# Kernel optimization log

Measured on AMD Instinct MI355X. Metric: run time of the kernel, lower is better.

Reference implementation:

```python
import jax, jax.numpy as jnp
import numpy as np

B, L, D, H = 2, 256, 256, 4
DH = D // H  # 64


def setup_inputs() -> dict:
    key = jax.random.key(0)
    ks = jax.random.split(key, 20)
    inp = {
        "q": jax.random.normal(ks[0], (B, L, D), jnp.float32),
        "k": jax.random.normal(ks[1], (B, L, D), jnp.float32),
        "v": jax.random.normal(ks[2], (B, L, D), jnp.float32),
        "attn_mask": jnp.zeros((L, L), jnp.float32),  # nonzero => masked
        "key_padding_mask": jnp.zeros((B, L), bool),
        "pitch_rel": jax.random.normal(ks[3], (B, L, L, D), jnp.float32),
        "dur_rel": jax.random.normal(ks[4], (B, L, L, D), jnp.float32),
    }
    scale = 1.0 / np.sqrt(D)
    names = ["Wq", "Wk", "Wv", "fc", "pr", "dr"]
    for i, n in enumerate(names):
        inp[n + "_w"] = jax.random.normal(ks[5 + 2 * i], (D, D), jnp.float32) * scale
        inp[n + "_b"] = jax.random.normal(ks[6 + 2 * i], (D,), jnp.float32) * 0.01
    return inp


def _linear(x, w, b):
    # torch nn.Linear: y = x @ W^T + b
    return jnp.matmul(x, w.T) + b


def reference(q, k, v, attn_mask, key_padding_mask, pitch_rel, dur_rel,
              Wq_w, Wq_b, Wk_w, Wk_b, Wv_w, Wv_b, fc_w, fc_b,
              pr_w, pr_b, dr_w, dr_b):
    Bq, Lq, Dm = q.shape
    Lk = k.shape[1]
    # project and split heads -> (B, H, L, DH)
    def heads(x, w, b):
        return _linear(x, w, b).reshape(Bq, -1, H, DH).transpose(0, 2, 1, 3)
    qh, kh, vh = heads(q, Wq_w, Wq_b), heads(k, Wk_w, Wk_b), heads(v, Wv_w, Wv_b)

    # content scores: (B, H, Lq, Lk)
    logits = jnp.einsum("bhid,bhjd->bhij", qh, kh)

    # relative pitch bias: pitch_rel (B, Lq, Lk, D) -> (B, Lq, Lk, H, DH)
    pr = _linear(pitch_rel, pr_w, pr_b).reshape(Bq, Lq, Lk, H, DH)
    logits = logits + jnp.einsum("bhid,bijhd->bhij", qh, pr)

    dr = _linear(dur_rel, dr_w, dr_b).reshape(Bq, Lq, Lk, H, DH)
    logits = logits + jnp.einsum("bhid,bijhd->bhij", qh, dr)

    logits = logits / np.sqrt(DH)

    # mask: key_padding_mask broadcast over the QUERY axis (as in source),
    # attn_mask nonzero => masked
    mask = jnp.logical_or(key_padding_mask[:, None, :, None],
                          (attn_mask != 0)[None, None, :, :])
    logits = jnp.where(mask, jnp.float32(-9e15), logits)

    attn = jax.nn.softmax(logits, axis=-1)  # (B, H, Lq, Lk)
    out = jnp.einsum("bhij,bhjd->bhid", attn, vh)  # (B, H, Lq, DH)
    out = out.transpose(0, 2, 1, 3).reshape(Bq, Lq, Dm)
    out = _linear(out, fc_w, fc_b)  # dropout is identity in eval mode
    return out, attn
```

## Files before the change

### kernel.cpp

```cpp
#include <hip/hip_runtime.h>
#include <math.h>


typedef float f4v __attribute__((ext_vector_type(4)));

#define SLD(dst, ptr)                                                     \
  asm volatile("global_load_dwordx4 %0, %1, off sc0 sc1 nt"               \
               : "=v"(dst)                                                \
               : "v"((unsigned long long)(const void*)(ptr))              \
               : "memory")

#define VW(n)                                             \
  asm volatile("s_waitcnt vmcnt(%0)" ::"i"(n) : "memory"); \
  __builtin_amdgcn_sched_barrier(0)

__global__ __launch_bounds__(256) void k_proj(
    const float* __restrict__ q, const float* __restrict__ k_, const float* __restrict__ v,
    const float* __restrict__ Wq, const float* __restrict__ Bq,
    const float* __restrict__ Wk, const float* __restrict__ Bk,
    const float* __restrict__ Wv, const float* __restrict__ Bv,
    float* __restrict__ qh, float* __restrict__ kh, float* __restrict__ vh) {
  int blk = blockIdx.x;
  int m = blk >> 5;
  int r = blk & 31;
  int b = r >> 4, it = (r >> 2) & 3, ot = r & 3;
  const float* X = (m == 0) ? q : (m == 1) ? k_ : v;
  const float* W = (m == 0) ? Wq : (m == 1) ? Wk : Wv;
  const float* Bs = (m == 0) ? Bq : (m == 1) ? Bk : Bv;
  float* OUT = (m == 0) ? qh : (m == 1) ? kh : vh;
  const float scale = (m == 0) ? 0.125f : 1.0f;

  __shared__ float xs[64][33];
  __shared__ float ws[64][33];
  int tid = threadIdx.x;
  int ti = tid >> 4, to = tid & 15;
  int lr = tid >> 2, lc = (tid & 3) * 8;
  float acc[4][4] = {};

  for (int k0 = 0; k0 < 256; k0 += 32) {
    float4 a0 = *(const float4*)(X + (size_t)(b * 256 + it * 64 + lr) * 256 + k0 + lc);
    float4 a1 = *(const float4*)(X + (size_t)(b * 256 + it * 64 + lr) * 256 + k0 + lc + 4);
    xs[lr][lc + 0] = a0.x; xs[lr][lc + 1] = a0.y; xs[lr][lc + 2] = a0.z; xs[lr][lc + 3] = a0.w;
    xs[lr][lc + 4] = a1.x; xs[lr][lc + 5] = a1.y; xs[lr][lc + 6] = a1.z; xs[lr][lc + 7] = a1.w;
    float4 w0 = *(const float4*)(W + (size_t)(ot * 64 + lr) * 256 + k0 + lc);
    float4 w1 = *(const float4*)(W + (size_t)(ot * 64 + lr) * 256 + k0 + lc + 4);
    ws[lr][lc + 0] = w0.x; ws[lr][lc + 1] = w0.y; ws[lr][lc + 2] = w0.z; ws[lr][lc + 3] = w0.w;
    ws[lr][lc + 4] = w1.x; ws[lr][lc + 5] = w1.y; ws[lr][lc + 6] = w1.z; ws[lr][lc + 7] = w1.w;
    __syncthreads();
#pragma unroll
    for (int kk = 0; kk < 32; ++kk) {
      float xv0 = xs[ti * 4 + 0][kk], xv1 = xs[ti * 4 + 1][kk];
      float xv2 = xs[ti * 4 + 2][kk], xv3 = xs[ti * 4 + 3][kk];
      float wv0 = ws[0 * 16 + to][kk], wv1 = ws[1 * 16 + to][kk];
      float wv2 = ws[2 * 16 + to][kk], wv3 = ws[3 * 16 + to][kk];
      acc[0][0] += xv0 * wv0; acc[0][1] += xv0 * wv1; acc[0][2] += xv0 * wv2; acc[0][3] += xv0 * wv3;
      acc[1][0] += xv1 * wv0; acc[1][1] += xv1 * wv1; acc[1][2] += xv1 * wv2; acc[1][3] += xv1 * wv3;
      acc[2][0] += xv2 * wv0; acc[2][1] += xv2 * wv1; acc[2][2] += xv2 * wv2; acc[2][3] += xv2 * wv3;
      acc[3][0] += xv3 * wv0; acc[3][1] += xv3 * wv1; acc[3][2] += xv3 * wv2; acc[3][3] += xv3 * wv3;
    }
    __syncthreads();
  }
#pragma unroll
  for (int ii = 0; ii < 4; ++ii)
#pragma unroll
    for (int oo = 0; oo < 4; ++oo) {
      int i = it * 64 + ti * 4 + ii;
      int dd = oo * 16 + to;
      OUT[(size_t)((b * 4 + ot) * 256 + i) * 64 + dd] = (acc[ii][oo] + Bs[ot * 64 + dd]) * scale;
    }
}

static __device__ void body_qprdr(int blk, const float* __restrict__ qh,
                                  const float* __restrict__ prw, const float* __restrict__ drw,
                                  float* __restrict__ qpr, float* __restrict__ qdr) {
  int t = blk >> 7;
  int r2 = blk & 127;
  int rt = r2 >> 2, et = r2 & 3;
  const float* W = t ? drw : prw;
  float* OUT = t ? qdr : qpr;
  int h = (rt >> 2) & 3;

  __shared__ float xs[64][33];
  __shared__ float ws2[32][64];
  int tid = threadIdx.x;
  int ti = tid >> 4, to = tid & 15;
  float acc[4][4] = {};

  for (int k0 = 0; k0 < 64; k0 += 32) {
    int lr = tid >> 2, lc = (tid & 3) * 8;
    float4 a0 = *(const float4*)(qh + (size_t)(rt * 64 + lr) * 64 + k0 + lc);
    float4 a1 = *(const float4*)(qh + (size_t)(rt * 64 + lr) * 64 + k0 + lc + 4);
    xs[lr][lc + 0] = a0.x; xs[lr][lc + 1] = a0.y; xs[lr][lc + 2] = a0.z; xs[lr][lc + 3] = a0.w;
    xs[lr][lc + 4] = a1.x; xs[lr][lc + 5] = a1.y; xs[lr][lc + 6] = a1.z; xs[lr][lc + 7] = a1.w;
    int wr = tid >> 3, wc = (tid & 7) * 8;
    float4 w0 = *(const float4*)(W + (size_t)(h * 64 + k0 + wr) * 256 + et * 64 + wc);
    float4 w1 = *(const float4*)(W + (size_t)(h * 64 + k0 + wr) * 256 + et * 64 + wc + 4);
    ws2[wr][wc + 0] = w0.x; ws2[wr][wc + 1] = w0.y; ws2[wr][wc + 2] = w0.z; ws2[wr][wc + 3] = w0.w;
    ws2[wr][wc + 4] = w1.x; ws2[wr][wc + 5] = w1.y; ws2[wr][wc + 6] = w1.z; ws2[wr][wc + 7] = w1.w;
    __syncthreads();
#pragma unroll
    for (int kk = 0; kk < 32; ++kk) {
      float xv0 = xs[ti * 4 + 0][kk], xv1 = xs[ti * 4 + 1][kk];
      float xv2 = xs[ti * 4 + 2][kk], xv3 = xs[ti * 4 + 3][kk];
      float wv0 = ws2[kk][0 * 16 + to], wv1 = ws2[kk][1 * 16 + to];
      float wv2 = ws2[kk][2 * 16 + to], wv3 = ws2[kk][3 * 16 + to];
      acc[0][0] += xv0 * wv0; acc[0][1] += xv0 * wv1; acc[0][2] += xv0 * wv2; acc[0][3] += xv0 * wv3;
      acc[1][0] += xv1 * wv0; acc[1][1] += xv1 * wv1; acc[1][2] += xv1 * wv2; acc[1][3] += xv1 * wv3;
      acc[2][0] += xv2 * wv0; acc[2][1] += xv2 * wv1; acc[2][2] += xv2 * wv2; acc[2][3] += xv2 * wv3;
      acc[3][0] += xv3 * wv0; acc[3][1] += xv3 * wv1; acc[3][2] += xv3 * wv2; acc[3][3] += xv3 * wv3;
    }
    __syncthreads();
  }
#pragma unroll
  for (int ii = 0; ii < 4; ++ii)
#pragma unroll
    for (int oo = 0; oo < 4; ++oo)
      OUT[(size_t)(rt * 64 + ti * 4 + ii) * 256 + et * 64 + oo * 16 + to] = acc[ii][oo];
}

static __device__ void body_qk(int blk, const float* __restrict__ qh,
                               const float* __restrict__ kh, float* __restrict__ qk) {
  int bh = blk >> 4, it = (blk >> 2) & 3, jt = blk & 3;
  __shared__ float xs[64][33];
  __shared__ float ys[64][33];
  int tid = threadIdx.x;
  int ti = tid >> 4, to = tid & 15;
  float acc[4][4] = {};

  for (int k0 = 0; k0 < 64; k0 += 32) {
    int lr = tid >> 2, lc = (tid & 3) * 8;
    float4 a0 = *(const float4*)(qh + (size_t)(bh * 256 + it * 64 + lr) * 64 + k0 + lc);
    float4 a1 = *(const float4*)(qh + (size_t)(bh * 256 + it * 64 + lr) * 64 + k0 + lc + 4);
    xs[lr][lc + 0] = a0.x; xs[lr][lc + 1] = a0.y; xs[lr][lc + 2] = a0.z; xs[lr][lc + 3] = a0.w;
    xs[lr][lc + 4] = a1.x; xs[lr][lc + 5] = a1.y; xs[lr][lc + 6] = a1.z; xs[lr][lc + 7] = a1.w;
    float4 b0 = *(const float4*)(kh + (size_t)(bh * 256 + jt * 64 + lr) * 64 + k0 + lc);
    float4 b1 = *(const float4*)(kh + (size_t)(bh * 256 + jt * 64 + lr) * 64 + k0 + lc + 4);
    ys[lr][lc + 0] = b0.x; ys[lr][lc + 1] = b0.y; ys[lr][lc + 2] = b0.z; ys[lr][lc + 3] = b0.w;
    ys[lr][lc + 4] = b1.x; ys[lr][lc + 5] = b1.y; ys[lr][lc + 6] = b1.z; ys[lr][lc + 7] = b1.w;
    __syncthreads();
#pragma unroll
    for (int kk = 0; kk < 32; ++kk) {
      float xv0 = xs[ti * 4 + 0][kk], xv1 = xs[ti * 4 + 1][kk];
      float xv2 = xs[ti * 4 + 2][kk], xv3 = xs[ti * 4 + 3][kk];
      float wv0 = ys[0 * 16 + to][kk], wv1 = ys[1 * 16 + to][kk];
      float wv2 = ys[2 * 16 + to][kk], wv3 = ys[3 * 16 + to][kk];
      acc[0][0] += xv0 * wv0; acc[0][1] += xv0 * wv1; acc[0][2] += xv0 * wv2; acc[0][3] += xv0 * wv3;
      acc[1][0] += xv1 * wv0; acc[1][1] += xv1 * wv1; acc[1][2] += xv1 * wv2; acc[1][3] += xv1 * wv3;
      acc[2][0] += xv2 * wv0; acc[2][1] += xv2 * wv1; acc[2][2] += xv2 * wv2; acc[2][3] += xv2 * wv3;
      acc[3][0] += xv3 * wv0; acc[3][1] += xv3 * wv1; acc[3][2] += xv3 * wv2; acc[3][3] += xv3 * wv3;
    }
    __syncthreads();
  }
#pragma unroll
  for (int ii = 0; ii < 4; ++ii)
#pragma unroll
    for (int jj = 0; jj < 4; ++jj)
      qk[(size_t)(bh * 256 + it * 64 + ti * 4 + ii) * 256 + jt * 64 + jj * 16 + to] = acc[ii][jj];
}

static __device__ void body_transpose(int blk, const float* __restrict__ in,
                                      float* __restrict__ out) {
  __shared__ float t[32][33];
  int bx = blk & 7, by = blk >> 3;
  int x = threadIdx.x & 31, y0 = threadIdx.x >> 5;
#pragma unroll
  for (int yy = 0; yy < 32; yy += 8)
    t[yy + y0][x] = in[(size_t)(by * 32 + yy + y0) * 256 + bx * 32 + x];
  __syncthreads();
#pragma unroll
  for (int yy = 0; yy < 32; yy += 8)
    out[(size_t)(bx * 32 + yy + y0) * 256 + by * 32 + x] = t[x][yy + y0];
}

__global__ __launch_bounds__(256) void k_mid(
    const float* __restrict__ qh, const float* __restrict__ kh,
    const float* __restrict__ prw, const float* __restrict__ drw,
    float* __restrict__ qpr, float* __restrict__ qdr, float* __restrict__ qk,
    const float* __restrict__ fcw, float* __restrict__ fcT) {
  int blk = blockIdx.x;
  if (blk < 256) body_qprdr(blk, qh, prw, drw, qpr, qdr);
  else if (blk < 384) body_qk(blk - 256, qh, kh, qk);
  else body_transpose(blk - 384, fcw, fcT);
}

__global__ __launch_bounds__(256, 4) void k_fused3(
    const float* __restrict__ pitch, const float* __restrict__ dur,
    const float* __restrict__ qpr, const float* __restrict__ qdr,
    const float* __restrict__ amask, const unsigned char* __restrict__ kpm,
    const float* __restrict__ vh, const float* __restrict__ fcT,
    const float* __restrict__ fcb, float* __restrict__ attn,
    float* __restrict__ out) {
  int bi = blockIdx.x;
  int b = bi >> 8, i = bi & 255;
  int tid = threadIdx.x, w = tid >> 6, l = tid & 63;
  int j0 = w * 64;

  __shared__ float red[4][4][4][65];
  __shared__ float logits[4][264];
  __shared__ float pre[256];

  float4 qp[4], qd[4];
#pragma unroll
  for (int h = 0; h < 4; ++h) {
    qp[h] = *(const float4*)(qpr + (size_t)((b * 4 + h) * 256 + i) * 256 + 4 * l);
    qd[h] = *(const float4*)(qdr + (size_t)((b * 4 + h) * 256 + i) * 256 + 4 * l);
  }

  float* qrow = attn + (size_t)((b * 4 + w) * 256 + i) * 256;
  float4 qk4 = *(const float4*)(qrow + 4 * l);
  float4 m4 = *(const float4*)(amask + (size_t)i * 256 + 4 * l);
  bool rowm = kpm[b * 256 + i] != 0;

  int p2 = l & 15, row_o = p2 >> 2, h_o = p2 & 3, sub = l >> 4;

  const float* pbase = pitch + ((size_t)bi * 256 + j0) * 256 + 4 * l;
  const float* dbase = dur + ((size_t)bi * 256 + j0) * 256 + 4 * l;

  asm volatile("s_waitcnt vmcnt(0)" ::: "memory");

  f4v PA[4], DA[4], PB[4], DB[4];

#define ISSUE(PP, DD, g)                                  \
  {                                                       \
    _Pragma("unroll") for (int r = 0; r < 4; ++r) {       \
      SLD(PP[r], pbase + ((g) * 4 + r) * 256);            \
      SLD(DD[r], dbase + ((g) * 4 + r) * 256);            \
    }                                                     \
  }

#define COMPUTE(PP, DD, g)                                                        \
  {                                                                               \
    _Pragma("unroll") for (int r = 0; r < 4; ++r) {                               \
      red[w][r][0][l] = PP[r].x * qp[0].x + PP[r].y * qp[0].y + PP[r].z * qp[0].z \
                      + PP[r].w * qp[0].w + DD[r].x * qd[0].x + DD[r].y * qd[0].y \
                      + DD[r].z * qd[0].z + DD[r].w * qd[0].w;                    \
      red[w][r][1][l] = PP[r].x * qp[1].x + PP[r].y * qp[1].y + PP[r].z * qp[1].z \
                      + PP[r].w * qp[1].w + DD[r].x * qd[1].x + DD[r].y * qd[1].y \
                      + DD[r].z * qd[1].z + DD[r].w * qd[1].w;                    \
      red[w][r][2][l] = PP[r].x * qp[2].x + PP[r].y * qp[2].y + PP[r].z * qp[2].z \
                      + PP[r].w * qp[2].w + DD[r].x * qd[2].x + DD[r].y * qd[2].y \
                      + DD[r].z * qd[2].z + DD[r].w * qd[2].w;                    \
      red[w][r][3][l] = PP[r].x * qp[3].x + PP[r].y * qp[3].y + PP[r].z * qp[3].z \
                      + PP[r].w * qp[3].w + DD[r].x * qd[3].x + DD[r].y * qd[3].y \
                      + DD[r].z * qd[3].z + DD[r].w * qd[3].w;                    \
    }                                                                             \
    float x = 0.f;                                                                \
    {                                                                             \
      const float* rr = &red[w][row_o][h_o][sub * 16];                            \
      _Pragma("unroll") for (int c = 0; c < 16; ++c) x += rr[c];                  \
    }                                                                             \
    x += __shfl_xor(x, 16);                                                       \
    x += __shfl_xor(x, 32);                                                       \
    if (l < 16) logits[h_o][j0 + (g) * 4 + row_o] = x;                            \
  }

  ISSUE(PA, DA, 0);
  ISSUE(PB, DB, 1);
#pragma unroll
  for (int gg = 0; gg < 8; ++gg) {
    VW(8);
    COMPUTE(PA, DA, 2 * gg);
    if (gg < 7) ISSUE(PA, DA, 2 * gg + 2);
    if (gg < 7) {
      VW(8);
    } else {
      VW(0);
    }
    COMPUTE(PB, DB, 2 * gg + 1);
    if (gg < 7) ISSUE(PB, DB, 2 * gg + 3);
  }
#undef ISSUE
#undef COMPUTE
  __syncthreads();

  float* lrow = &logits[w][0];
  float4 bv = *(float4*)(lrow + 4 * l);
  float v0 = (rowm || m4.x != 0.f) ? -9e15f : qk4.x + bv.x;
  float v1 = (rowm || m4.y != 0.f) ? -9e15f : qk4.y + bv.y;
  float v2 = (rowm || m4.z != 0.f) ? -9e15f : qk4.z + bv.z;
  float v3 = (rowm || m4.w != 0.f) ? -9e15f : qk4.w + bv.w;

  float mx = fmaxf(fmaxf(v0, v1), fmaxf(v2, v3));
#pragma unroll
  for (int m = 1; m <= 32; m <<= 1) mx = fmaxf(mx, __shfl_xor(mx, m));
  float e0 = __expf(v0 - mx), e1 = __expf(v1 - mx);
  float e2 = __expf(v2 - mx), e3 = __expf(v3 - mx);
  float sm = e0 + e1 + e2 + e3;
#pragma unroll
  for (int m = 1; m <= 32; m <<= 1) sm += __shfl_xor(sm, m);
  float inv = 1.0f / sm;
  float4 a4 = make_float4(e0 * inv, e1 * inv, e2 * inv, e3 * inv);
  *(float4*)(qrow + 4 * l) = a4;
  *(float4*)(lrow + 4 * l) = a4;

  float acc = 0.f;
  const float* vbase = vh + (size_t)(b * 4 + w) * 256 * 64 + l;
#pragma unroll 4
  for (int jj = 0; jj < 256; ++jj) acc += lrow[jj] * vbase[(size_t)jj * 64];
  pre[tid] = acc;
  __syncthreads();

  float acc2 = fcb[tid];
#pragma unroll 4
  for (int c = 0; c < 256; ++c) acc2 += pre[c] * fcT[(size_t)c * 256 + tid];
  out[(size_t)(b * 256 + i) * 256 + tid] = acc2;
}

extern "C" void kernel_launch(void* const* d_in, const int* in_sizes, int n_in,
                              void* d_out, int out_size, void* d_ws, size_t ws_size,
                              hipStream_t stream) {
  (void)in_sizes; (void)n_in; (void)out_size; (void)ws_size;
  const float* q = (const float*)d_in[0];
  const float* k = (const float*)d_in[1];
  const float* v = (const float*)d_in[2];
  const float* amask = (const float*)d_in[3];
  const unsigned char* kpm = (const unsigned char*)d_in[4];
  const float* pitch = (const float*)d_in[5];
  const float* dur = (const float*)d_in[6];
  const float* Wq = (const float*)d_in[7];
  const float* Bq = (const float*)d_in[8];
  const float* Wk = (const float*)d_in[9];
  const float* Bk = (const float*)d_in[10];
  const float* Wv = (const float*)d_in[11];
  const float* Bv = (const float*)d_in[12];
  const float* fcw = (const float*)d_in[13];
  const float* fcb = (const float*)d_in[14];
  const float* prw = (const float*)d_in[15];
  const float* drw = (const float*)d_in[17];

  float* out = (float*)d_out;
  float* attn = out + 2 * 256 * 256;

  float* wsf = (float*)d_ws;
  float* qh = wsf;
  float* kh = qh + 131072;
  float* vh = kh + 131072;
  float* qpr = vh + 131072;
  float* qdr = qpr + 524288;
  float* fcT = qdr + 524288;

  k_proj<<<96, 256, 0, stream>>>(q, k, v, Wq, Bq, Wk, Bk, Wv, Bv, qh, kh, vh);
  k_mid<<<448, 256, 0, stream>>>(qh, kh, prw, drw, qpr, qdr, attn, fcw, fcT);
  k_fused3<<<512, 256, 0, stream>>>(pitch, dur, qpr, qdr, amask, kpm, vh, fcT, fcb, attn, out);
}
```

Baseline: 108.1 us.

## Fuse q·Wpr/q·Wdr and QK^T computation into main attention kernel, drop mid launch

Removes the middle kernel that precomputed q-projected pitch/duration weights and QK^T into global memory. Each block of the main kernel now computes its own qpr/qdr rows (q times the relevant weight slice) and its QK^T row directly from qh/kh, staging the projected vectors in shared memory it reuses. The fc transpose moves into the projection kernel. This saves one launch and the global round-trip of the intermediates, but the weight products are now recomputed per block, with extra loads and syncs before the streaming loop. Launch bounds drop from 4 to 2 waves per SIMD target.

```diff
diff --git a/kernel.cpp b/kernel.cpp
--- a/kernel.cpp
+++ b/kernel.cpp
@@ -14,13 +14,12 @@
   asm volatile("s_waitcnt vmcnt(%0)" ::"i"(n) : "memory"); \
   __builtin_amdgcn_sched_barrier(0)
 
-__global__ __launch_bounds__(256) void k_proj(
-    const float* __restrict__ q, const float* __restrict__ k_, const float* __restrict__ v,
-    const float* __restrict__ Wq, const float* __restrict__ Bq,
+static __device__ void body_proj(
+    int blk, const float* __restrict__ q, const float* __restrict__ k_,
+    const float* __restrict__ v, const float* __restrict__ Wq, const float* __restrict__ Bq,
     const float* __restrict__ Wk, const float* __restrict__ Bk,
     const float* __restrict__ Wv, const float* __restrict__ Bv,
     float* __restrict__ qh, float* __restrict__ kh, float* __restrict__ vh) {
-  int blk = blockIdx.x;
   int m = blk >> 5;
   int r = blk & 31;
   int b = r >> 4, it = (r >> 2) & 3, ot = r & 3;
@@ -70,94 +69,6 @@
     }
 }
 
-static __device__ void body_qprdr(int blk, const float* __restrict__ qh,
-                                  const float* __restrict__ prw, const float* __restrict__ drw,
-                                  float* __restrict__ qpr, float* __restrict__ qdr) {
-  int t = blk >> 7;
-  int r2 = blk & 127;
-  int rt = r2 >> 2, et = r2 & 3;
-  const float* W = t ? drw : prw;
-  float* OUT = t ? qdr : qpr;
-  int h = (rt >> 2) & 3;
-
-  __shared__ float xs[64][33];
-  __shared__ float ws2[32][64];
-  int tid = threadIdx.x;
-  int ti = tid >> 4, to = tid & 15;
-  float acc[4][4] = {};
-
-  for (int k0 = 0; k0 < 64; k0 += 32) {
-    int lr = tid >> 2, lc = (tid & 3) * 8;
-    float4 a0 = *(const float4*)(qh + (size_t)(rt * 64 + lr) * 64 + k0 + lc);
-    float4 a1 = *(const float4*)(qh + (size_t)(rt * 64 + lr) * 64 + k0 + lc + 4);
-    xs[lr][lc + 0] = a0.x; xs[lr][lc + 1] = a0.y; xs[lr][lc + 2] = a0.z; xs[lr][lc + 3] = a0.w;
-    xs[lr][lc + 4] = a1.x; xs[lr][lc + 5] = a1.y; xs[lr][lc + 6] = a1.z; xs[lr][lc + 7] = a1.w;
-    int wr = tid >> 3, wc = (tid & 7) * 8;
-    float4 w0 = *(const float4*)(W + (size_t)(h * 64 + k0 + wr) * 256 + et * 64 + wc);
-    float4 w1 = *(const float4*)(W + (size_t)(h * 64 + k0 + wr) * 256 + et * 64 + wc + 4);
-    ws2[wr][wc + 0] = w0.x; ws2[wr][wc + 1] = w0.y; ws2[wr][wc + 2] = w0.z; ws2[wr][wc + 3] = w0.w;
-    ws2[wr][wc + 4] = w1.x; ws2[wr][wc + 5] = w1.y; ws2[wr][wc + 6] = w1.z; ws2[wr][wc + 7] = w1.w;
-    __syncthreads();
-#pragma unroll
-    for (int kk = 0; kk < 32; ++kk) {
-      float xv0 = xs[ti * 4 + 0][kk], xv1 = xs[ti * 4 + 1][kk];
-      float xv2 = xs[ti * 4 + 2][kk], xv3 = xs[ti * 4 + 3][kk];
-      float wv0 = ws2[kk][0 * 16 + to], wv1 = ws2[kk][1 * 16 + to];
-      float wv2 = ws2[kk][2 * 16 + to], wv3 = ws2[kk][3 * 16 + to];
-      acc[0][0] += xv0 * wv0; acc[0][1] += xv0 * wv1; acc[0][2] += xv0 * wv2; acc[0][3] += xv0 * wv3;
-      acc[1][0] += xv1 * wv0; acc[1][1] += xv1 * wv1; acc[1][2] += xv1 * wv2; acc[1][3] += xv1 * wv3;
-      acc[2][0] += xv2 * wv0; acc[2][1] += xv2 * wv1; acc[2][2] += xv2 * wv2; acc[2][3] += xv2 * wv3;
-      acc[3][0] += xv3 * wv0; acc[3][1] += xv3 * wv1; acc[3][2] += xv3 * wv2; acc[3][3] += xv3 * wv3;
-    }
-    __syncthreads();
-  }
-#pragma unroll
-  for (int ii = 0; ii < 4; ++ii)
-#pragma unroll
-    for (int oo = 0; oo < 4; ++oo)
-      OUT[(size_t)(rt * 64 + ti * 4 + ii) * 256 + et * 64 + oo * 16 + to] = acc[ii][oo];
-}
-
-static __device__ void body_qk(int blk, const float* __restrict__ qh,
-                               const float* __restrict__ kh, float* __restrict__ qk) {
-  int bh = blk >> 4, it = (blk >> 2) & 3, jt = blk & 3;
-  __shared__ float xs[64][33];
-  __shared__ float ys[64][33];
-  int tid = threadIdx.x;
-  int ti = tid >> 4, to = tid & 15;
-  float acc[4][4] = {};
-
-  for (int k0 = 0; k0 < 64; k0 += 32) {
-    int lr = tid >> 2, lc = (tid & 3) * 8;
-    float4 a0 = *(const float4*)(qh + (size_t)(bh * 256 + it * 64 + lr) * 64 + k0 + lc);
-    float4 a1 = *(const float4*)(qh + (size_t)(bh * 256 + it * 64 + lr) * 64 + k0 + lc + 4);
-    xs[lr][lc + 0] = a0.x; xs[lr][lc + 1] = a0.y; xs[lr][lc + 2] = a0.z; xs[lr][lc + 3] = a0.w;
-    xs[lr][lc + 4] = a1.x; xs[lr][lc + 5] = a1.y; xs[lr][lc + 6] = a1.z; xs[lr][lc + 7] = a1.w;
-    float4 b0 = *(const float4*)(kh + (size_t)(bh * 256 + jt * 64 + lr) * 64 + k0 + lc);
-    float4 b1 = *(const float4*)(kh + (size_t)(bh * 256 + jt * 64 + lr) * 64 + k0 + lc + 4);
-    ys[lr][lc + 0] = b0.x; ys[lr][lc + 1] = b0.y; ys[lr][lc + 2] = b0.z; ys[lr][lc + 3] = b0.w;
-    ys[lr][lc + 4] = b1.x; ys[lr][lc + 5] = b1.y; ys[lr][lc + 6] = b1.z; ys[lr][lc + 7] = b1.w;
-    __syncthreads();
-#pragma unroll
-    for (int kk = 0; kk < 32; ++kk) {
-      float xv0 = xs[ti * 4 + 0][kk], xv1 = xs[ti * 4 + 1][kk];
-      float xv2 = xs[ti * 4 + 2][kk], xv3 = xs[ti * 4 + 3][kk];
-      float wv0 = ys[0 * 16 + to][kk], wv1 = ys[1 * 16 + to][kk];
-      float wv2 = ys[2 * 16 + to][kk], wv3 = ys[3 * 16 + to][kk];
-      acc[0][0] += xv0 * wv0; acc[0][1] += xv0 * wv1; acc[0][2] += xv0 * wv2; acc[0][3] += xv0 * wv3;
-      acc[1][0] += xv1 * wv0; acc[1][1] += xv1 * wv1; acc[1][2] += xv1 * wv2; acc[1][3] += xv1 * wv3;
-      acc[2][0] += xv2 * wv0; acc[2][1] += xv2 * wv1; acc[2][2] += xv2 * wv2; acc[2][3] += xv2 * wv3;
-      acc[3][0] += xv3 * wv0; acc[3][1] += xv3 * wv1; acc[3][2] += xv3 * wv2; acc[3][3] += xv3 * wv3;
-    }
-    __syncthreads();
-  }
-#pragma unroll
-  for (int ii = 0; ii < 4; ++ii)
-#pragma unroll
-    for (int jj = 0; jj < 4; ++jj)
-      qk[(size_t)(bh * 256 + it * 64 + ti * 4 + ii) * 256 + jt * 64 + jj * 16 + to] = acc[ii][jj];
-}
-
 static __device__ void body_transpose(int blk, const float* __restrict__ in,
                                       float* __restrict__ out) {
   __shared__ float t[32][33];
@@ -172,20 +83,22 @@
     out[(size_t)(bx * 32 + yy + y0) * 256 + by * 32 + x] = t[x][yy + y0];
 }
 
-__global__ __launch_bounds__(256) void k_mid(
+__global__ __launch_bounds__(256) void k_proj(
+    const float* __restrict__ q, const float* __restrict__ k_, const float* __restrict__ v,
+    const float* __restrict__ Wq, const float* __restrict__ Bq,
+    const float* __restrict__ Wk, const float* __restrict__ Bk,
+    const float* __restrict__ Wv, const float* __restrict__ Bv,
+    float* __restrict__ qh, float* __restrict__ kh, float* __restrict__ vh,
+    const float* __restrict__ fcw, float* __restrict__ fcT) {
+  int blk = blockIdx.x;
+  if (blk < 96) body_proj(blk, q, k_, v, Wq, Bq, Wk, Bk, Wv, Bv, qh, kh, vh);
+  else body_transpose(blk - 96, fcw, fcT);
+}
+
+__global__ __launch_bounds__(256, 2) void k_fused4(
+    const float* __restrict__ pitch, const float* __restrict__ dur,
     const float* __restrict__ qh, const float* __restrict__ kh,
     const float* __restrict__ prw, const float* __restrict__ drw,
-    float* __restrict__ qpr, float* __restrict__ qdr, float* __restrict__ qk,
-    const float* __restrict__ fcw, float* __restrict__ fcT) {
-  int blk = blockIdx.x;
-  if (blk < 256) body_qprdr(blk, qh, prw, drw, qpr, qdr);
-  else if (blk < 384) body_qk(blk - 256, qh, kh, qk);
-  else body_transpose(blk - 384, fcw, fcT);
-}
-
-__global__ __launch_bounds__(256, 4) void k_fused3(
-    const float* __restrict__ pitch, const float* __restrict__ dur,
-    const float* __restrict__ qpr, const float* __restrict__ qdr,
     const float* __restrict__ amask, const unsigned char* __restrict__ kpm,
     const float* __restrict__ vh, const float* __restrict__ fcT,
     const float* __restrict__ fcb, float* __restrict__ attn,
@@ -199,24 +112,62 @@
   __shared__ float logits[4][264];
   __shared__ float pre[256];
 
-  float4 qp[4], qd[4];
-#pragma unroll
-  for (int h = 0; h < 4; ++h) {
-    qp[h] = *(const float4*)(qpr + (size_t)((b * 4 + h) * 256 + i) * 256 + 4 * l);
-    qd[h] = *(const float4*)(qdr + (size_t)((b * 4 + h) * 256 + i) * 256 + 4 * l);
-  }
-
-  float* qrow = attn + (size_t)((b * 4 + w) * 256 + i) * 256;
-  float4 qk4 = *(const float4*)(qrow + 4 * l);
+  logits[w][l] = qh[((size_t)(b * 4 + w) * 256 + i) * 64 + l];
+
+  float* qprs = &red[0][0][0][0];
+  float* qdrs = qprs + 1024;
+  {
+    const float* pw = prw + (size_t)(w * 64) * 256 + 4 * l;
+    const float* dw = drw + (size_t)(w * 64) * 256 + 4 * l;
+    float4 ap = make_float4(0.f, 0.f, 0.f, 0.f);
+    float4 ad = make_float4(0.f, 0.f, 0.f, 0.f);
+#pragma unroll 8
+    for (int d = 0; d < 64; ++d) {
+      float qv = logits[w][d];
+      float4 pv = *(const float4*)(pw + d * 256);
+      float4 dv = *(const float4*)(dw + d * 256);
+      ap.x += qv * pv.x; ap.y += qv * pv.y; ap.z += qv * pv.z; ap.w += qv * pv.w;
+      ad.x += qv * dv.x; ad.y += qv * dv.y; ad.z += qv * dv.z; ad.w += qv * dv.w;
+    }
+    *(float4*)&qprs[w * 256 + 4 * l] = ap;
+    *(float4*)&qdrs[w * 256 + 4 * l] = ad;
+  }
+
+  float4 qk4;
+  {
+    const float* khb = kh + (size_t)((b * 4 + w) * 256) * 64;
+    float a0 = 0.f, a1 = 0.f, a2 = 0.f, a3 = 0.f;
+#pragma unroll 4
+    for (int c = 0; c < 16; ++c) {
+      float4 qv = *(const float4*)&logits[w][4 * c];
+      float4 k0 = *(const float4*)(khb + (size_t)(4 * l + 0) * 64 + 4 * c);
+      float4 k1 = *(const float4*)(khb + (size_t)(4 * l + 1) * 64 + 4 * c);
+      float4 k2 = *(const float4*)(khb + (size_t)(4 * l + 2) * 64 + 4 * c);
+      float4 k3 = *(const float4*)(khb + (size_t)(4 * l + 3) * 64 + 4 * c);
+      a0 += k0.x * qv.x + k0.y * qv.y + k0.z * qv.z + k0.w * qv.w;
+      a1 += k1.x * qv.x + k1.y * qv.y + k1.z * qv.z + k1.w * qv.w;
+      a2 += k2.x * qv.x + k2.y * qv.y + k2.z * qv.z + k2.w * qv.w;
+      a3 += k3.x * qv.x + k3.y * qv.y + k3.z * qv.z + k3.w * qv.w;
+    }
+    qk4 = make_float4(a0, a1, a2, a3);
+  }
+
   float4 m4 = *(const float4*)(amask + (size_t)i * 256 + 4 * l);
   bool rowm = kpm[b * 256 + i] != 0;
 
+  __syncthreads();
+  float4 qp[4], qd[4];
+#pragma unroll
+  for (int h = 0; h < 4; ++h) {
+    qp[h] = *(const float4*)&qprs[h * 256 + 4 * l];
+    qd[h] = *(const float4*)&qdrs[h * 256 + 4 * l];
+  }
+  __syncthreads();
+
   int p2 = l & 15, row_o = p2 >> 2, h_o = p2 & 3, sub = l >> 4;
 
   const float* pbase = pitch + ((size_t)bi * 256 + j0) * 256 + 4 * l;
   const float* dbase = dur + ((size_t)bi * 256 + j0) * 256 + 4 * l;
-
-  asm volatile("s_waitcnt vmcnt(0)" ::: "memory");
 
   f4v PA[4], DA[4], PB[4], DB[4];
 
@@ -274,6 +225,7 @@
   __syncthreads();
 
   float* lrow = &logits[w][0];
+  float* qrow = attn + (size_t)((b * 4 + w) * 256 + i) * 256;
   float4 bv = *(float4*)(lrow + 4 * l);
   float v0 = (rowm || m4.x != 0.f) ? -9e15f : qk4.x + bv.x;
   float v1 = (rowm || m4.y != 0.f) ? -9e15f : qk4.y + bv.y;
@@ -335,11 +287,9 @@
   float* qh = wsf;
   float* kh = qh + 131072;
   float* vh = kh + 131072;
-  float* qpr = vh + 131072;
-  float* qdr = qpr + 524288;
-  float* fcT = qdr + 524288;
-
-  k_proj<<<96, 256, 0, stream>>>(q, k, v, Wq, Bq, Wk, Bk, Wv, Bv, qh, kh, vh);
-  k_mid<<<448, 256, 0, stream>>>(qh, kh, prw, drw, qpr, qdr, attn, fcw, fcT);
-  k_fused3<<<512, 256, 0, stream>>>(pitch, dur, qpr, qdr, amask, kpm, vh, fcT, fcb, attn, out);
-}
+  float* fcT = vh + 131072;
+
+  k_proj<<<160, 256, 0, stream>>>(q, k, v, Wq, Bq, Wk, Bk, Wv, Bv, qh, kh, vh, fcw, fcT);
+  k_fused4<<<512, 256, 0, stream>>>(pitch, dur, qh, kh, prw, drw, amask, kpm, vh, fcT,
+                                    fcb, attn, out);
+}
```

Result: slower. 112.5 us (+4.0%).
